# Optimization experiments

Hardware: AMD Instinct MI355X
Metric: run time of the kernel (lower is better)

The kernel has to match this reference:

```python
import jax, jax.numpy as jnp
import numpy as np

D_MODEL = 1024
N_HEADS = 16
HEAD_DIM = D_MODEL // N_HEADS
D_C = 128
THETA = 10000.0


def rope_cos_sin(timestamps):
    # timestamps: (B, L) -> cos, sin: (B, L, HEAD_DIM)
    freqs = 1.0 / (THETA ** (jnp.arange(0, HEAD_DIM, 2, dtype=jnp.float32) / HEAD_DIM))
    t = timestamps[..., None] * freqs            # (B, L, HEAD_DIM//2)
    emb = jnp.concatenate([t, t], axis=-1)       # (B, L, HEAD_DIM)
    return jnp.cos(emb), jnp.sin(emb)


def rotate_half(x):
    x1, x2 = jnp.split(x, 2, axis=-1)
    return jnp.concatenate([-x2, x1], axis=-1)


def setup_inputs() -> dict:
    key = jax.random.key(0)
    ks = jax.random.split(key, 10)
    B, L = 2, 2048
    s = 0.02
    return {
        "query": jax.random.normal(ks[0], (B, L, D_MODEL), jnp.float32),
        "timestamps_q": jax.random.uniform(ks[1], (B, L), jnp.float32) * 365.0,
        "timestamps_kv": jax.random.uniform(ks[2], (B, L), jnp.float32) * 365.0,
        "w_kv_c": jax.random.normal(ks[3], (D_MODEL, D_C), jnp.float32) * s,
        "w_kc_up": jax.random.normal(ks[4], (D_C, D_MODEL), jnp.float32) * s,
        "w_vc_up": jax.random.normal(ks[5], (D_C, D_MODEL), jnp.float32) * s,
        "w_qr": jax.random.normal(ks[6], (D_MODEL, D_MODEL), jnp.float32) * s,
        "w_kr": jax.random.normal(ks[7], (D_MODEL, D_MODEL), jnp.float32) * s,
        "w_o": jax.random.normal(ks[8], (D_MODEL, D_MODEL), jnp.float32) * s,
    }


def reference(query, timestamps_q, timestamps_kv, w_kv_c, w_kc_up, w_vc_up, w_qr, w_kr, w_o):
    B, Lq, _ = query.shape
    key_value = query  # self-attention path (key_value defaults to query)
    Lk = key_value.shape[1]

    def heads(x, L):  # (B, L, D) -> (B, H, L, hd)
        return x.reshape(B, L, N_HEADS, HEAD_DIM).transpose(0, 2, 1, 3)

    c_kv = key_value @ w_kv_c                      # (B, Lk, d_c) low-rank KV
    k_c = heads(c_kv @ w_kc_up, Lk)
    v_c = heads(c_kv @ w_vc_up, Lk)
    q_r = heads(query @ w_qr, Lq)
    k_r = heads(key_value @ w_kr, Lk)

    cos_q, _ = rope_cos_sin(timestamps_q)
    cos_k, _ = rope_cos_sin(timestamps_kv)
    cos_q = cos_q[:, None]                          # (B, 1, Lq, hd)
    cos_k = cos_k[:, None]                          # (B, 1, Lk, hd)
    # Faithful to original (which passes cos_k in the `sin` slot):
    q_r = q_r * cos_q + rotate_half(q_r) * cos_k
    k_r = k_r * cos_q + rotate_half(k_r) * cos_k

    scale = HEAD_DIM ** -0.5
    qs = q_r * scale
    attn = jnp.einsum("bhqd,bhkd->bhqk", qs, k_c) + jnp.einsum("bhqd,bhkd->bhqk", qs, k_r)
    attn_weights = jax.nn.softmax(attn, axis=-1)
    out = jnp.einsum("bhqk,bhkd->bhqd", attn_weights, v_c)
    out = out.transpose(0, 2, 1, 3).reshape(B, Lq, D_MODEL)
    return out @ w_o
```

## Files before the change

kernel.cpp:

```cpp
#include <hip/hip_runtime.h>

typedef float          f32x4    __attribute__((ext_vector_type(4)));
typedef float          float8v  __attribute__((ext_vector_type(8)));
typedef unsigned short ushort8v __attribute__((ext_vector_type(8)));
typedef __bf16         bf16x8   __attribute__((ext_vector_type(8)));

__device__ __forceinline__ unsigned short f2b(float x) {
  union { __bf16 b; unsigned short u; } v;
  v.b = (__bf16)x;
  return v.u;
}
__device__ __forceinline__ float b2f(unsigned short h) {
  union { unsigned u; float f; } v; v.u = ((unsigned)h) << 16;
  return v.f;
}

__device__ __forceinline__ void g2lds16(const unsigned short* g,
                                        unsigned short* l) {
  __builtin_amdgcn_global_load_lds(
      (const __attribute__((address_space(1))) unsigned int*)g,
      (__attribute__((address_space(3))) unsigned int*)l, 16, 0, 0);
}

__global__ void cvt_kernel(const float* __restrict__ src,
                           unsigned short* __restrict__ dst, int n8) {
  int i = blockIdx.x * 256 + threadIdx.x;
  if (i >= n8) return;
  float8v v = reinterpret_cast<const float8v*>(src)[i];
  ushort8v h;
#pragma unroll
  for (int j = 0; j < 8; ++j) h[j] = f2b(v[j]);
  reinterpret_cast<ushort8v*>(dst)[i] = h;
}

__global__ __launch_bounds__(256) void wtrans_kernel(
    const float* __restrict__ W, unsigned short* __restrict__ WT,
    int K, int N) {
  __shared__ unsigned short T[64 * 72];
  const int tid = threadIdx.x;
  const int n0 = blockIdx.x * 64, k0 = blockIdx.y * 64;
#pragma unroll
  for (int it = 0; it < 2; ++it) {
    int c = tid + it * 256;
    int r = c >> 3, cc = c & 7;
    float8v v = *reinterpret_cast<const float8v*>(
        &W[(size_t)(k0 + r) * N + n0 + cc * 8]);
    ushort8v h;
#pragma unroll
    for (int j = 0; j < 8; ++j) h[j] = f2b(v[j]);
    *reinterpret_cast<ushort8v*>(&T[r * 72 + cc * 8]) = h;
  }
  __syncthreads();
#pragma unroll
  for (int it = 0; it < 2; ++it) {
    int c = tid + it * 256;
    int n = c >> 3, kc = c & 7;
    ushort8v y;
#pragma unroll
    for (int j = 0; j < 8; ++j) y[j] = T[(kc * 8 + j) * 72 + n];
    *reinterpret_cast<ushort8v*>(&WT[(size_t)(n0 + n) * K + k0 + kc * 8]) = y;
  }
}

template <int TM, typename CT, bool ACC>
__global__ __launch_bounds__(256) void gemm_bt(
    const unsigned short* __restrict__ A, const unsigned short* __restrict__ Bt,
    CT* __restrict__ C, int M, int N, int K) {
  __shared__ unsigned short As[TM * 64];
  __shared__ unsigned short Bs[128 * 64];
  const int tid = threadIdx.x;
  const int m0 = blockIdx.y * TM, n0 = blockIdx.x * 128;
  const int wave = tid >> 6, lane = tid & 63;
  const int wm = (wave >> 1) * (TM / 2), wn = (wave & 1) * 64;
  const int l16 = lane & 15, quad = lane >> 4;
  constexpr int MI = TM / 32;

  f32x4 acc[MI][4];
#pragma unroll
  for (int i = 0; i < MI; ++i)
#pragma unroll
    for (int j = 0; j < 4; ++j)
#pragma unroll
      for (int r = 0; r < 4; ++r) acc[i][j][r] = 0.f;

  for (int k0 = 0; k0 < K; k0 += 64) {
    __syncthreads();
#pragma unroll
    for (int it = 0; it < TM * 8 / 256; ++it) {
      int c = it * 256 + tid;
      int m = c >> 3, kc = (c & 7) ^ (m & 7);
      g2lds16(&A[(size_t)(m0 + m) * K + k0 + kc * 8], &As[c * 8]);
    }
#pragma unroll
    for (int it = 0; it < 4; ++it) {
      int c = it * 256 + tid;
      int n = c >> 3, kc = (c & 7) ^ (n & 7);
      g2lds16(&Bt[(size_t)(n0 + n) * K + k0 + kc * 8], &Bs[c * 8]);
    }
    __syncthreads();

#pragma unroll
    for (int ks = 0; ks < 2; ++ks) {
      bf16x8 af[MI], bfr[4];
#pragma unroll
      for (int mi = 0; mi < MI; ++mi) {
        int m = wm + mi * 16 + l16;
        af[mi] = *reinterpret_cast<const bf16x8*>(
            &As[(m * 8 + ((ks * 4 + quad) ^ (m & 7))) * 8]);
      }
#pragma unroll
      for (int ni = 0; ni < 4; ++ni) {
        int n = wn + ni * 16 + l16;
        bfr[ni] = *reinterpret_cast<const bf16x8*>(
            &Bs[(n * 8 + ((ks * 4 + quad) ^ (n & 7))) * 8]);
      }
#pragma unroll
      for (int mi = 0; mi < MI; ++mi)
#pragma unroll
        for (int ni = 0; ni < 4; ++ni)
          acc[mi][ni] = __builtin_amdgcn_mfma_f32_16x16x32_bf16(
              af[mi], bfr[ni], acc[mi][ni], 0, 0, 0);
    }
  }

#pragma unroll
  for (int mi = 0; mi < MI; ++mi)
#pragma unroll
    for (int ni = 0; ni < 4; ++ni) {
      int row = m0 + wm + mi * 16 + quad * 4;
      int col = n0 + wn + ni * 16 + l16;
#pragma unroll
      for (int r = 0; r < 4; ++r) {
        size_t idx = (size_t)(row + r) * N + col;
        float val = acc[mi][ni][r];
        if constexpr (sizeof(CT) == 2) {
          if constexpr (ACC) val += b2f(C[idx]);
          C[idx] = f2b(val);
        } else {
          if constexpr (ACC) val += C[idx];
          C[idx] = val;
        }
      }
    }
}

__global__ __launch_bounds__(256) void gemm_fused3(
    const unsigned short* __restrict__ A, const unsigned short* __restrict__ Bt,
    unsigned short* __restrict__ Cq, unsigned short* __restrict__ Ck,
    unsigned short* __restrict__ Cc, int K) {
  __shared__ unsigned short As[1024 * 8];
  __shared__ unsigned short Bs[1024 * 8];
  const int tid = threadIdx.x;
  const int m0 = blockIdx.y * 128, n0 = blockIdx.x * 128;
  const int wave = tid >> 6, lane = tid & 63;
  const int wm = (wave >> 1) * 64, wn = (wave & 1) * 64;
  const int l16 = lane & 15, quad = lane >> 4;

  f32x4 acc[4][4];
#pragma unroll
  for (int i = 0; i < 4; ++i)
#pragma unroll
    for (int j = 0; j < 4; ++j)
#pragma unroll
      for (int r = 0; r < 4; ++r) acc[i][j][r] = 0.f;

  for (int k0 = 0; k0 < K; k0 += 64) {
    __syncthreads();
#pragma unroll
    for (int it = 0; it < 4; ++it) {
      int c = it * 256 + tid;
      int m = c >> 3, kc = (c & 7) ^ (m & 7);
      g2lds16(&A[(size_t)(m0 + m) * K + k0 + kc * 8], &As[c * 8]);
    }
#pragma unroll
    for (int it = 0; it < 4; ++it) {
      int c = it * 256 + tid;
      int n = c >> 3, kc = (c & 7) ^ (n & 7);
      g2lds16(&Bt[(size_t)(n0 + n) * K + k0 + kc * 8], &Bs[c * 8]);
    }
    __syncthreads();

#pragma unroll
    for (int ks = 0; ks < 2; ++ks) {
      bf16x8 af[4], bfr[4];
#pragma unroll
      for (int mi = 0; mi < 4; ++mi) {
        int m = wm + mi * 16 + l16;
        af[mi] = *reinterpret_cast<const bf16x8*>(
            &As[(m * 8 + ((ks * 4 + quad) ^ (m & 7))) * 8]);
      }
#pragma unroll
      for (int ni = 0; ni < 4; ++ni) {
        int n = wn + ni * 16 + l16;
        bfr[ni] = *reinterpret_cast<const bf16x8*>(
            &Bs[(n * 8 + ((ks * 4 + quad) ^ (n & 7))) * 8]);
      }
#pragma unroll
      for (int mi = 0; mi < 4; ++mi)
#pragma unroll
        for (int ni = 0; ni < 4; ++ni)
          acc[mi][ni] = __builtin_amdgcn_mfma_f32_16x16x32_bf16(
              af[mi], bfr[ni], acc[mi][ni], 0, 0, 0);
    }
  }

  unsigned short* dst;
  int w, cb;
  if (n0 < 1024)      { dst = Cq; w = 1024; cb = 0; }
  else if (n0 < 2048) { dst = Ck; w = 1024; cb = 1024; }
  else                { dst = Cc; w = 128;  cb = 2048; }
#pragma unroll
  for (int mi = 0; mi < 4; ++mi)
#pragma unroll
    for (int ni = 0; ni < 4; ++ni) {
      int row = m0 + wm + mi * 16 + quad * 4;
      int col = n0 - cb + wn + ni * 16 + l16;
#pragma unroll
      for (int r = 0; r < 4; ++r)
        dst[(size_t)(row + r) * w + col] = f2b(acc[mi][ni][r]);
    }
}

__global__ __launch_bounds__(256) void gemm_fused2(
    const unsigned short* __restrict__ A, const unsigned short* __restrict__ Bt,
    unsigned short* __restrict__ Ck, unsigned short* __restrict__ Cv, int K) {
  __shared__ unsigned short As[1024 * 8];
  __shared__ unsigned short Bs[1024 * 8];
  const int tid = threadIdx.x;
  const int m0 = blockIdx.y * 128, n0 = blockIdx.x * 128;
  const int wave = tid >> 6, lane = tid & 63;
  const int wm = (wave >> 1) * 64, wn = (wave & 1) * 64;
  const int l16 = lane & 15, quad = lane >> 4;

  f32x4 acc[4][4];
#pragma unroll
  for (int i = 0; i < 4; ++i)
#pragma unroll
    for (int j = 0; j < 4; ++j)
#pragma unroll
      for (int r = 0; r < 4; ++r) acc[i][j][r] = 0.f;

  for (int k0 = 0; k0 < K; k0 += 64) {
    __syncthreads();
#pragma unroll
    for (int it = 0; it < 4; ++it) {
      int c = it * 256 + tid;
      int m = c >> 3, kc = (c & 7) ^ (m & 7);
      g2lds16(&A[(size_t)(m0 + m) * K + k0 + kc * 8], &As[c * 8]);
    }
#pragma unroll
    for (int it = 0; it < 4; ++it) {
      int c = it * 256 + tid;
      int n = c >> 3, kc = (c & 7) ^ (n & 7);
      g2lds16(&Bt[(size_t)(n0 + n) * K + k0 + kc * 8], &Bs[c * 8]);
    }
    __syncthreads();

#pragma unroll
    for (int ks = 0; ks < 2; ++ks) {
      bf16x8 af[4], bfr[4];
#pragma unroll
      for (int mi = 0; mi < 4; ++mi) {
        int m = wm + mi * 16 + l16;
        af[mi] = *reinterpret_cast<const bf16x8*>(
            &As[(m * 8 + ((ks * 4 + quad) ^ (m & 7))) * 8]);
      }
#pragma unroll
      for (int ni = 0; ni < 4; ++ni) {
        int n = wn + ni * 16 + l16;
        bfr[ni] = *reinterpret_cast<const bf16x8*>(
            &Bs[(n * 8 + ((ks * 4 + quad) ^ (n & 7))) * 8]);
      }
#pragma unroll
      for (int mi = 0; mi < 4; ++mi)
#pragma unroll
        for (int ni = 0; ni < 4; ++ni)
          acc[mi][ni] = __builtin_amdgcn_mfma_f32_16x16x32_bf16(
              af[mi], bfr[ni], acc[mi][ni], 0, 0, 0);
    }
  }

  const bool first = (n0 < 1024);
  unsigned short* dst = first ? Ck : Cv;
  int cb = first ? 0 : 1024;
#pragma unroll
  for (int mi = 0; mi < 4; ++mi)
#pragma unroll
    for (int ni = 0; ni < 4; ++ni) {
      int row = m0 + wm + mi * 16 + quad * 4;
      int col = n0 - cb + wn + ni * 16 + l16;
#pragma unroll
      for (int r = 0; r < 4; ++r) {
        size_t idx = (size_t)(row + r) * 1024 + col;
        float val = acc[mi][ni][r];
        if (first) val += b2f(dst[idx]);
        dst[idx] = f2b(val);
      }
    }
}

__global__ void rope_kernel(unsigned short* __restrict__ qr,
                            unsigned short* __restrict__ kr,
                            const float* __restrict__ tq,
                            const float* __restrict__ tk) {
  int idx = blockIdx.x * 256 + threadIdx.x;
  int i = idx & 31;
  int mh = idx >> 5;
  int m = mh >> 4;
  float f = exp2f(-(float)i * (13.287712379549449f / 32.f));
  float cq = cosf(tq[m] * f);
  float ck = cosf(tk[m] * f);
  size_t base = (size_t)mh * 64;
  const float qscale = 0.18033688011112042f;
  float q1 = b2f(qr[base + i]), q2 = b2f(qr[base + i + 32]);
  float k1 = b2f(kr[base + i]), k2 = b2f(kr[base + i + 32]);
  qr[base + i]      = f2b((q1 * cq - q2 * ck) * qscale);
  qr[base + i + 32] = f2b((q2 * cq + q1 * ck) * qscale);
  kr[base + i]      = f2b(k1 * cq - k2 * ck);
  kr[base + i + 32] = f2b(k2 * cq + k1 * ck);
}

__global__ __launch_bounds__(256) void vtrans_kernel(
    const unsigned short* __restrict__ v, unsigned short* __restrict__ vt,
    int L) {
  __shared__ unsigned short T[64 * 72];
  const int tid = threadIdx.x;
  const int l0 = blockIdx.x * 64, bh = blockIdx.y;
  const size_t inbase = ((size_t)(bh >> 4) * L) * 1024 + (bh & 15) * 64;
  const size_t outbase = (size_t)bh * 64 * L;
#pragma unroll
  for (int it = 0; it < 2; ++it) {
    int c = tid + it * 256;
    int l = c >> 3, dc = c & 7;
    ushort8v x = *reinterpret_cast<const ushort8v*>(
        &v[inbase + (size_t)(l0 + l) * 1024 + dc * 8]);
    *reinterpret_cast<ushort8v*>(&T[l * 72 + dc * 8]) = x;
  }
  __syncthreads();
#pragma unroll
  for (int it = 0; it < 2; ++it) {
    int c = tid + it * 256;
    int d = c >> 3, g = c & 7;
    ushort8v y;
#pragma unroll
    for (int e = 0; e < 8; ++e) {
      int k = ((g >> 2) << 5) | ((e >> 2) << 4) | (((g >> 1) & 1) << 3) |
              ((g & 1) << 2) | (e & 3);
      y[e] = T[k * 72 + d];
    }
    *reinterpret_cast<ushort8v*>(&vt[outbase + (size_t)d * L + l0 + g * 8]) = y;
  }
}

__global__ __launch_bounds__(256) void flash14_kernel(
    const unsigned short* __restrict__ qs, const unsigned short* __restrict__ ks,
    const unsigned short* __restrict__ vt, unsigned short* __restrict__ o,
    int L) {
  __shared__ unsigned short Ks[2][512 * 8];
  __shared__ unsigned short Vs[2][512 * 8];
  const int tid = threadIdx.x;
  const int wave = tid >> 6, lane = tid & 63;
  const int l16 = lane & 15, quad = lane >> 4;
  const int bh = blockIdx.y;
  const int qb = blockIdx.x * 128 + wave * 32;
  const size_t base = ((size_t)(bh >> 4) * L) * 1024 + (bh & 15) * 64;
  const size_t vtbase = (size_t)bh * 64 * L;

  bf16x8 aq[2][2];
#pragma unroll
  for (int mt = 0; mt < 2; ++mt) {
    size_t qrow = base + (size_t)(qb + mt * 16 + l16) * 1024;
    aq[mt][0] = *reinterpret_cast<const bf16x8*>(&qs[qrow + quad * 8]);
    aq[mt][1] = *reinterpret_cast<const bf16x8*>(&qs[qrow + 32 + quad * 8]);
  }

  ushort8v onesu;
#pragma unroll
  for (int j = 0; j < 8; ++j) onesu[j] = 0x3F80;
  bf16x8 ones = *reinterpret_cast<bf16x8*>(&onesu);

  f32x4 oacc[2][4];
  f32x4 lacc[2];
#pragma unroll
  for (int mt = 0; mt < 2; ++mt) {
#pragma unroll
    for (int r = 0; r < 4; ++r) lacc[mt][r] = 0.f;
#pragma unroll
    for (int nt = 0; nt < 4; ++nt)
#pragma unroll
      for (int r = 0; r < 4; ++r) oacc[mt][nt][r] = 0.f;
  }

  const int T = L / 64;
#pragma unroll
  for (int it = 0; it < 2; ++it) {
    int c = it * 256 + tid;
    int key = c >> 3, dc = (c & 7) ^ (key & 7);
    g2lds16(&ks[base + (size_t)key * 1024 + dc * 8], &Ks[0][c * 8]);
  }
#pragma unroll
  for (int it = 0; it < 2; ++it) {
    int c = it * 256 + tid;
    int d = c >> 3, kc = (c & 7) ^ (d & 7);
    g2lds16(&vt[vtbase + (size_t)d * L + kc * 8], &Vs[0][c * 8]);
  }

  for (int t = 0; t < T; ++t) {
    __syncthreads();
    if (t + 1 < T) {
      int k0 = (t + 1) * 64, nb = (t + 1) & 1;
#pragma unroll
      for (int it = 0; it < 2; ++it) {
        int c = it * 256 + tid;
        int key = c >> 3, dc = (c & 7) ^ (key & 7);
        g2lds16(&ks[base + (size_t)(k0 + key) * 1024 + dc * 8], &Ks[nb][c * 8]);
      }
#pragma unroll
      for (int it = 0; it < 2; ++it) {
        int c = it * 256 + tid;
        int d = c >> 3, kc = (c & 7) ^ (d & 7);
        g2lds16(&vt[vtbase + (size_t)d * L + k0 + kc * 8], &Vs[nb][c * 8]);
      }
    }
    const int cb = t & 1;

    f32x4 st[2][4];
#pragma unroll
    for (int nt = 0; nt < 4; ++nt) {
      int key = nt * 16 + l16;
      int dc0 = quad ^ (key & 7);
      int dc1 = (4 + quad) ^ (key & 7);
      bf16x8 bk0 = *reinterpret_cast<const bf16x8*>(
          &Ks[cb][(key * 8 + dc0) * 8]);
      bf16x8 bk1 = *reinterpret_cast<const bf16x8*>(
          &Ks[cb][(key * 8 + dc1) * 8]);
#pragma unroll
      for (int mt = 0; mt < 2; ++mt) {
        f32x4 z; z[0] = z[1] = z[2] = z[3] = 0.f;
        z = __builtin_amdgcn_mfma_f32_16x16x32_bf16(bk0, aq[mt][0], z, 0, 0, 0);
        z = __builtin_amdgcn_mfma_f32_16x16x32_bf16(bk1, aq[mt][1], z, 0, 0, 0);
        st[mt][nt] = z;
      }
    }

    bf16x8 ap[2][2];
#pragma unroll
    for (int mt = 0; mt < 2; ++mt) {
#pragma unroll
      for (int hf = 0; hf < 2; ++hf)
#pragma unroll
        for (int w = 0; w < 4; ++w) {
          int nt = 2 * hf + (w >> 1), p = w & 1;
          ap[mt][hf][2 * w] =
              (__bf16)__builtin_amdgcn_exp2f(st[mt][nt][2 * p]);
          ap[mt][hf][2 * w + 1] =
              (__bf16)__builtin_amdgcn_exp2f(st[mt][nt][2 * p + 1]);
        }
      lacc[mt] = __builtin_amdgcn_mfma_f32_16x16x32_bf16(ap[mt][0], ones,
                                                         lacc[mt], 0, 0, 0);
      lacc[mt] = __builtin_amdgcn_mfma_f32_16x16x32_bf16(ap[mt][1], ones,
                                                         lacc[mt], 0, 0, 0);
    }

#pragma unroll
    for (int nt = 0; nt < 4; ++nt) {
      int d = nt * 16 + l16;
#pragma unroll
      for (int hf = 0; hf < 2; ++hf) {
        int kc = (hf * 4 + quad) ^ (d & 7);
        bf16x8 bv = *reinterpret_cast<const bf16x8*>(
            &Vs[cb][(d * 8 + kc) * 8]);
#pragma unroll
        for (int mt = 0; mt < 2; ++mt)
          oacc[mt][nt] = __builtin_amdgcn_mfma_f32_16x16x32_bf16(
              ap[mt][hf], bv, oacc[mt][nt], 0, 0, 0);
      }
    }
  }

#pragma unroll
  for (int mt = 0; mt < 2; ++mt)
#pragma unroll
    for (int r = 0; r < 4; ++r) {
      float inv = __builtin_amdgcn_rcpf(lacc[mt][r]);
      int q = qb + mt * 16 + quad * 4 + r;
#pragma unroll
      for (int nt = 0; nt < 4; ++nt)
        o[base + (size_t)q * 1024 + nt * 16 + l16] =
            f2b(oacc[mt][nt][r] * inv);
    }
}

extern "C" void kernel_launch(void* const* d_in, const int* in_sizes, int n_in,
                              void* d_out, int out_size, void* d_ws, size_t ws_size,
                              hipStream_t stream) {
  const float* X    = (const float*)d_in[0];
  const float* tq   = (const float*)d_in[1];
  const float* tk   = (const float*)d_in[2];
  const float* wkvc = (const float*)d_in[3];
  const float* wkc  = (const float*)d_in[4];
  const float* wvc  = (const float*)d_in[5];
  const float* wqr  = (const float*)d_in[6];
  const float* wkr  = (const float*)d_in[7];
  const float* wo   = (const float*)d_in[8];

  const int D = 1024, DC = 128, L = 2048;
  const int M = in_sizes[0] / D;
  const int B = M / L;
  const int NBH = B * 16;
  (void)n_in; (void)out_size; (void)ws_size;

  unsigned short* p = (unsigned short*)d_ws;
  auto take = [&](size_t n) { unsigned short* r = p; p += n; return r; };
  unsigned short* Xb    = take((size_t)M * D);
  unsigned short* qsb   = take((size_t)M * D);
  unsigned short* ksb   = take((size_t)M * D);
  unsigned short* vcb   = take((size_t)M * D);
  unsigned short* ckv   = take((size_t)M * DC);
  unsigned short* Wbig  = take((size_t)(2 * D + DC) * D);
  unsigned short* Wkcvc = take((size_t)(2 * D) * DC);
  unsigned short* WoT   = take((size_t)D * D);
  unsigned short* vtb   = Xb;
  unsigned short* obuf  = vcb;

  cvt_kernel<<<(M * D / 8 + 255) / 256, 256, 0, stream>>>(X, Xb, M * D / 8);
  auto wt = [&](const float* W, unsigned short* WT, int K, int N) {
    dim3 g(N / 64, K / 64);
    wtrans_kernel<<<g, 256, 0, stream>>>(W, WT, K, N);
  };
  wt(wqr,  Wbig,                          D, D);
  wt(wkr,  Wbig + (size_t)D * D,          D, D);
  wt(wkvc, Wbig + (size_t)2 * D * D,      D, DC);
  wt(wkc,  Wkcvc,                         DC, D);
  wt(wvc,  Wkcvc + (size_t)D * DC,        DC, D);
  wt(wo,   WoT,                           D, D);

  {
    dim3 g((2 * D + DC) / 128, M / 128);
    gemm_fused3<<<g, 256, 0, stream>>>(Xb, Wbig, qsb, ksb, ckv, D);
  }
  rope_kernel<<<(M * 512) / 256, 256, 0, stream>>>(qsb, ksb, tq, tk);
  {
    dim3 g(2 * D / 128, M / 128);
    gemm_fused2<<<g, 256, 0, stream>>>(ckv, Wkcvc, ksb, vcb, DC);
  }

  dim3 tg(L / 64, NBH);
  vtrans_kernel<<<tg, 256, 0, stream>>>(vcb, vtb, L);

  dim3 fg(L / 128, NBH);
  flash14_kernel<<<fg, 256, 0, stream>>>(qsb, ksb, vtb, obuf, L);

  {
    dim3 g(D / 128, M / 64);
    gemm_bt<64, float, false><<<g, 256, 0, stream>>>(
        obuf, WoT, (float*)d_out, M, D, D);
  }
}
```

Baseline: 226.0 us.

## Split key range across two wave groups in flash kernel and merge partials

```diff
diff --git a/kernel.cpp b/kernel.cpp
--- a/kernel.cpp
+++ b/kernel.cpp
@@ -352,19 +352,21 @@
   }
 }
 
-__global__ __launch_bounds__(256) void flash14_kernel(
+__global__ __launch_bounds__(512) void flash15_kernel(
     const unsigned short* __restrict__ qs, const unsigned short* __restrict__ ks,
     const unsigned short* __restrict__ vt, unsigned short* __restrict__ o,
     int L) {
-  __shared__ unsigned short Ks[2][512 * 8];
-  __shared__ unsigned short Vs[2][512 * 8];
+  __shared__ unsigned short KV[2][2][2][512 * 8];
   const int tid = threadIdx.x;
   const int wave = tid >> 6, lane = tid & 63;
+  const int half = wave >> 2;
   const int l16 = lane & 15, quad = lane >> 4;
   const int bh = blockIdx.y;
-  const int qb = blockIdx.x * 128 + wave * 32;
+  const int qb = blockIdx.x * 128 + (wave & 3) * 32;
   const size_t base = ((size_t)(bh >> 4) * L) * 1024 + (bh & 15) * 64;
   const size_t vtbase = (size_t)bh * 64 * L;
+  const int kvoff = half * (L >> 1);
+  const int sid = tid & 255;
 
   bf16x8 aq[2][2];
 #pragma unroll
@@ -391,38 +393,44 @@
       for (int r = 0; r < 4; ++r) oacc[mt][nt][r] = 0.f;
   }
 
-  const int T = L / 64;
+  const int T = L / 128;
 #pragma unroll
   for (int it = 0; it < 2; ++it) {
-    int c = it * 256 + tid;
+    int c = it * 256 + sid;
     int key = c >> 3, dc = (c & 7) ^ (key & 7);
-    g2lds16(&ks[base + (size_t)key * 1024 + dc * 8], &Ks[0][c * 8]);
+    g2lds16(&ks[base + (size_t)(kvoff + key) * 1024 + dc * 8],
+            &KV[0][half][0][c * 8]);
   }
 #pragma unroll
   for (int it = 0; it < 2; ++it) {
-    int c = it * 256 + tid;
+    int c = it * 256 + sid;
     int d = c >> 3, kc = (c & 7) ^ (d & 7);
-    g2lds16(&vt[vtbase + (size_t)d * L + kc * 8], &Vs[0][c * 8]);
+    g2lds16(&vt[vtbase + (size_t)d * L + kvoff + kc * 8],
+            &KV[1][half][0][c * 8]);
   }
 
   for (int t = 0; t < T; ++t) {
     __syncthreads();
     if (t + 1 < T) {
-      int k0 = (t + 1) * 64, nb = (t + 1) & 1;
+      int k0 = kvoff + (t + 1) * 64, nb = (t + 1) & 1;
 #pragma unroll
       for (int it = 0; it < 2; ++it) {
-        int c = it * 256 + tid;
+        int c = it * 256 + sid;
         int key = c >> 3, dc = (c & 7) ^ (key & 7);
-        g2lds16(&ks[base + (size_t)(k0 + key) * 1024 + dc * 8], &Ks[nb][c * 8]);
+        g2lds16(&ks[base + (size_t)(k0 + key) * 1024 + dc * 8],
+                &KV[0][half][nb][c * 8]);
       }
 #pragma unroll
       for (int it = 0; it < 2; ++it) {
-        int c = it * 256 + tid;
+        int c = it * 256 + sid;
         int d = c >> 3, kc = (c & 7) ^ (d & 7);
-        g2lds16(&vt[vtbase + (size_t)d * L + k0 + kc * 8], &Vs[nb][c * 8]);
+        g2lds16(&vt[vtbase + (size_t)d * L + k0 + kc * 8],
+                &KV[1][half][nb][c * 8]);
       }
     }
     const int cb = t & 1;
+    const unsigned short* Ks = &KV[0][half][cb][0];
+    const unsigned short* Vs = &KV[1][half][cb][0];
 
     f32x4 st[2][4];
 #pragma unroll
@@ -430,10 +438,8 @@
       int key = nt * 16 + l16;
       int dc0 = quad ^ (key & 7);
       int dc1 = (4 + quad) ^ (key & 7);
-      bf16x8 bk0 = *reinterpret_cast<const bf16x8*>(
-          &Ks[cb][(key * 8 + dc0) * 8]);
-      bf16x8 bk1 = *reinterpret_cast<const bf16x8*>(
-          &Ks[cb][(key * 8 + dc1) * 8]);
+      bf16x8 bk0 = *reinterpret_cast<const bf16x8*>(&Ks[(key * 8 + dc0) * 8]);
+      bf16x8 bk1 = *reinterpret_cast<const bf16x8*>(&Ks[(key * 8 + dc1) * 8]);
 #pragma unroll
       for (int mt = 0; mt < 2; ++mt) {
         f32x4 z; z[0] = z[1] = z[2] = z[3] = 0.f;
@@ -468,8 +474,7 @@
 #pragma unroll
       for (int hf = 0; hf < 2; ++hf) {
         int kc = (hf * 4 + quad) ^ (d & 7);
-        bf16x8 bv = *reinterpret_cast<const bf16x8*>(
-            &Vs[cb][(d * 8 + kc) * 8]);
+        bf16x8 bv = *reinterpret_cast<const bf16x8*>(&Vs[(d * 8 + kc) * 8]);
 #pragma unroll
         for (int mt = 0; mt < 2; ++mt)
           oacc[mt][nt] = __builtin_amdgcn_mfma_f32_16x16x32_bf16(
@@ -478,17 +483,47 @@
     }
   }
 
-#pragma unroll
-  for (int mt = 0; mt < 2; ++mt)
-#pragma unroll
-    for (int r = 0; r < 4; ++r) {
-      float inv = __builtin_amdgcn_rcpf(lacc[mt][r]);
-      int q = qb + mt * 16 + quad * 4 + r;
+  __syncthreads();
+  float* cbuf = (float*)&KV[0][0][0][0];
+  if (half == 1) {
+    int slot = ((wave - 4) * 64 + lane) * 44;
+#pragma unroll
+    for (int mt = 0; mt < 2; ++mt) {
 #pragma unroll
       for (int nt = 0; nt < 4; ++nt)
-        o[base + (size_t)q * 1024 + nt * 16 + l16] =
-            f2b(oacc[mt][nt][r] * inv);
-    }
+        *reinterpret_cast<f32x4*>(&cbuf[slot + (mt * 4 + nt) * 4]) =
+            oacc[mt][nt];
+      *reinterpret_cast<f32x4*>(&cbuf[slot + 32 + mt * 4]) = lacc[mt];
+    }
+  }
+  __syncthreads();
+  if (half == 0) {
+    int slot = (wave * 64 + lane) * 44;
+#pragma unroll
+    for (int mt = 0; mt < 2; ++mt) {
+#pragma unroll
+      for (int nt = 0; nt < 4; ++nt) {
+        f32x4 ov = *reinterpret_cast<const f32x4*>(
+            &cbuf[slot + (mt * 4 + nt) * 4]);
+#pragma unroll
+        for (int r = 0; r < 4; ++r) oacc[mt][nt][r] += ov[r];
+      }
+      f32x4 lv = *reinterpret_cast<const f32x4*>(&cbuf[slot + 32 + mt * 4]);
+#pragma unroll
+      for (int r = 0; r < 4; ++r) lacc[mt][r] += lv[r];
+    }
+#pragma unroll
+    for (int mt = 0; mt < 2; ++mt)
+#pragma unroll
+      for (int r = 0; r < 4; ++r) {
+        float inv = __builtin_amdgcn_rcpf(lacc[mt][r]);
+        int q = qb + mt * 16 + quad * 4 + r;
+#pragma unroll
+        for (int nt = 0; nt < 4; ++nt)
+          o[base + (size_t)q * 1024 + nt * 16 + l16] =
+              f2b(oacc[mt][nt][r] * inv);
+      }
+  }
 }
 
 extern "C" void kernel_launch(void* const* d_in, const int* in_sizes, int n_in,
@@ -549,7 +584,7 @@
   vtrans_kernel<<<tg, 256, 0, stream>>>(vcb, vtb, L);
 
   dim3 fg(L / 128, NBH);
-  flash14_kernel<<<fg, 256, 0, stream>>>(qsb, ksb, vtb, obuf, L);
+  flash15_kernel<<<fg, 512, 0, stream>>>(qsb, ksb, vtb, obuf, L);
 
   {
     dim3 g(D / 128, M / 64);
```

Result: no change. 222.0 us (-1.8%).
